# Kernel optimization log

Measured on AMD Instinct MI355X. Metric: run time of the kernel, lower is better.

The kernel has to match this reference:

```python
import jax, jax.numpy as jnp
import numpy as np

B, LQ = 16, 2048
EMB1, EMB2, HDIM, NHEAD = 1024, 768, 1024, 16


def setup_inputs() -> dict:
    key = jax.random.key(0)
    ks = jax.random.split(key, 8)
    s1 = 1.0 / np.sqrt(EMB1)
    s2 = 1.0 / np.sqrt(EMB2)
    return {
        "emb1": jax.random.normal(ks[0], (B, LQ, EMB1), jnp.float32),
        "emb2": jax.random.normal(ks[1], (B, EMB2), jnp.float32),
        "Wq": jax.random.uniform(ks[2], (HDIM, EMB1), jnp.float32, -s1, s1),
        "bq": jax.random.uniform(ks[3], (HDIM,), jnp.float32, -s1, s1),
        "Wk": jax.random.uniform(ks[4], (HDIM, EMB2), jnp.float32, -s2, s2),
        "bk": jax.random.uniform(ks[5], (HDIM,), jnp.float32, -s2, s2),
        "Wv": jax.random.uniform(ks[6], (HDIM, EMB2), jnp.float32, -s2, s2),
        "bv": jax.random.uniform(ks[7], (HDIM,), jnp.float32, -s2, s2),
        "n_head": NHEAD,
    }


def reference(emb1, emb2, Wq, bq, Wk, bk, Wv, bv, n_head):
    b, lq, _ = emb1.shape
    hdim = Wq.shape[0]
    dh = hdim // n_head
    # Q: [b, lq, hdim] -> [b, H, lq, dh]
    q = (jnp.einsum("bqe,he->bqh", emb1, Wq) + bq).reshape(b, lq, n_head, dh).transpose(0, 2, 1, 3)
    # K, V from per-batch vector: [b, hdim] -> [b, H, 1, dh]
    k = (emb2 @ Wk.T + bk).reshape(b, 1, n_head, dh).transpose(0, 2, 1, 3)
    v = (emb2 @ Wv.T + bv).reshape(b, 1, n_head, dh).transpose(0, 2, 1, 3)
    # att: [b, H, lq, 1] (no softmax, no scaling)
    att = jnp.einsum("bhqd,bhkd->bhqk", q, k)
    # sigmoid gate broadcast-multiplied with V: [b,H,lq,1]*[b,H,1,dh] -> [b,H,lq,dh]
    out = jax.nn.sigmoid(att) * v
    # back to [b, lq, hdim]; torch .squeeze(1) is a no-op for lq > 1
    return out.transpose(0, 2, 1, 3).reshape(b, lq, hdim)
```

## Files before the change

kernel.cpp:

```cpp
#include <hip/hip_runtime.h>
#include <hip/hip_fp16.h>
#include <cstdint>


typedef float    f4v __attribute__((ext_vector_type(4)));
typedef _Float16 h8v __attribute__((ext_vector_type(8)));

__global__ __launch_bounds__(256) void kv_kernel(
    const float* __restrict__ emb2, const float* __restrict__ Wk,
    const float* __restrict__ bk,   const float* __restrict__ Wv,
    const float* __restrict__ bv,   float* __restrict__ ws)
{
    const int kind  = blockIdx.y;
    const int htile = blockIdx.x;
    const float* W    = kind ? Wv : Wk;
    const float* bias = kind ? bv : bk;
    float* outp = ws + (kind ? 16384 : 0);

    const int t  = threadIdx.x;
    const int es = t >> 6;
    const int hl = (t >> 4) & 3;
    const int b  = t & 15;
    const int h  = htile * 4 + hl;

    const float4* W4 = (const float4*)(W + (size_t)h * 768) + es * 48;
    const float4* E4 = (const float4*)(emb2 + (size_t)b * 768) + es * 48;

    float acc = 0.f;
    #pragma unroll 8
    for (int j = 0; j < 48; ++j) {
        float4 w = W4[j];
        float4 a = E4[j];
        acc += w.x * a.x + w.y * a.y + w.z * a.z + w.w * a.w;
    }

    __shared__ float red[256];
    red[t] = acc;
    __syncthreads();
    if (t < 64) {
        float s = red[t] + red[t + 64] + red[t + 128] + red[t + 192] + bias[h];
        outp[b * 1024 + h] = s;
    }
}

__global__ __launch_bounds__(256) void fold_kernel(
    const float* __restrict__ Wq, const float* __restrict__ bq,
    float* __restrict__ ws)
{
    const int h = blockIdx.x;
    const int b = blockIdx.y;
    const float* kvec = ws;
    float* attb = ws + 32768;
    __half* wqk = (__half*)((char*)ws + 132096);

    const int t = threadIdx.x;
    __shared__ float kk[64];
    if (t < 64) {
        float kvl = kvec[b * 1024 + h * 64 + t];
        kk[t] = kvl;
        float s = kvl * bq[h * 64 + t];
        s += __shfl_xor(s, 1);  s += __shfl_xor(s, 2);
        s += __shfl_xor(s, 4);  s += __shfl_xor(s, 8);
        s += __shfl_xor(s, 16); s += __shfl_xor(s, 32);
        if (t == 0) attb[b * 16 + h] = s;
    }
    __syncthreads();

    float4 acc = make_float4(0.f, 0.f, 0.f, 0.f);
    const float4* Wrow = (const float4*)(Wq + (size_t)(h * 64) * 1024) + t;
    #pragma unroll 8
    for (int d = 0; d < 64; ++d) {
        float4 w = Wrow[(size_t)d * 256];
        float kd = kk[d];
        acc.x += kd * w.x; acc.y += kd * w.y;
        acc.z += kd * w.z; acc.w += kd * w.w;
    }
    union { __half2 h2[2]; uint2 u; } pk;
    pk.h2[0] = __floats2half2_rn(acc.x, acc.y);
    pk.h2[1] = __floats2half2_rn(acc.z, acc.w);
    *(uint2*)(wqk + (size_t)(b * 16 + h) * 1024 + t * 4) = pk.u;
}

__global__ __launch_bounds__(128) void att_kernel(
    const float* __restrict__ emb1, const float* __restrict__ ws,
    float* __restrict__ out)
{
    const int b    = blockIdx.y;
    const int t    = threadIdx.x;
    const int w    = t >> 6;
    const int lane = t & 63;
    const int q    = lane >> 4;
    const int m    = lane & 15;

    const int row0 = blockIdx.x * 32 + w * 16;

    const float*    vvec  = ws + 16384 + b * 1024;
    const float*    attbp = ws + 32768 + b * 16;
    const _Float16* wqk   = (const _Float16*)((const char*)ws + 132096)
                          + (size_t)b * 16384;

    const float*    Ap = emb1 + ((size_t)b * 2048 + row0 + m) * 1024 + q * 8;
    const _Float16* Bp = wqk + m * 1024 + q * 8;

    f4v acc = {0.f, 0.f, 0.f, 0.f};

    f4v a0 = *(const f4v*)(Ap);
    f4v a1 = *(const f4v*)(Ap + 4);
    h8v bf = *(const h8v*)(Bp);

    for (int c = 0; c < 32; ++c) {
        const int cn = (c < 31) ? c + 1 : 31;
        const float* An = Ap + cn * 32;
        f4v a0n = *(const f4v*)(An);
        f4v a1n = *(const f4v*)(An + 4);
        h8v bfn = *(const h8v*)(Bp + cn * 32);

        h8v af;
        af[0] = (_Float16)a0[0]; af[1] = (_Float16)a0[1];
        af[2] = (_Float16)a0[2]; af[3] = (_Float16)a0[3];
        af[4] = (_Float16)a1[0]; af[5] = (_Float16)a1[1];
        af[6] = (_Float16)a1[2]; af[7] = (_Float16)a1[3];

        acc = __builtin_amdgcn_mfma_f32_16x16x32_f16(af, bf, acc, 0, 0, 0);

        a0 = a0n; a1 = a1n; bf = bfn;
    }

    __shared__ float gl[2][16 * 17];
    float* g = gl[w];
    const float attb_l = attbp[m];
    #pragma unroll
    for (int j = 0; j < 4; ++j) {
        float att  = acc[j] + attb_l;
        float gate = 1.0f / (1.0f + __expf(-att));
        g[(q * 4 + j) * 17 + m] = gate;
    }
    __syncthreads();

    f4v vv[4];
    #pragma unroll
    for (int s = 0; s < 4; ++s)
        vv[s] = *(const f4v*)(vvec + s * 256 + lane * 4);

    float* Ob = out + ((size_t)b * 2048 + row0) * 1024 + lane * 4;
    #pragma unroll
    for (int r = 0; r < 16; ++r) {
        #pragma unroll
        for (int s = 0; s < 4; ++s) {
            float gg = g[r * 17 + s * 4 + q];
            f4v o = gg * vv[s];
            __builtin_nontemporal_store(o, (f4v*)(Ob + (size_t)r * 1024 + s * 256));
        }
    }
}

extern "C" void kernel_launch(void* const* d_in, const int* in_sizes, int n_in,
                              void* d_out, int out_size, void* d_ws, size_t ws_size,
                              hipStream_t stream) {
    const float* emb1 = (const float*)d_in[0];
    const float* emb2 = (const float*)d_in[1];
    const float* Wq   = (const float*)d_in[2];
    const float* bq   = (const float*)d_in[3];
    const float* Wk   = (const float*)d_in[4];
    const float* bk   = (const float*)d_in[5];
    const float* Wv   = (const float*)d_in[6];
    const float* bv   = (const float*)d_in[7];
    float* out = (float*)d_out;
    float* ws  = (float*)d_ws;

    kv_kernel  <<<dim3(256, 2), 256, 0, stream>>>(emb2, Wk, bk, Wv, bv, ws);
    fold_kernel<<<dim3(16, 16), 256, 0, stream>>>(Wq, bq, ws);
    att_kernel <<<dim3(64, 16), 128, 0, stream>>>(emb1, ws, out);
}
```

Baseline: 285.3 us.

## Split att_kernel K-reduction across four waves with all loads issued upfront

```diff
diff --git a/kernel.cpp b/kernel.cpp
--- a/kernel.cpp
+++ b/kernel.cpp
@@ -81,7 +81,7 @@
     *(uint2*)(wqk + (size_t)(b * 16 + h) * 1024 + t * 4) = pk.u;
 }
 
-__global__ __launch_bounds__(128) void att_kernel(
+__global__ __launch_bounds__(256, 4) void att_kernel(
     const float* __restrict__ emb1, const float* __restrict__ ws,
     float* __restrict__ out)
 {
@@ -92,7 +92,8 @@
     const int q    = lane >> 4;
     const int m    = lane & 15;
 
-    const int row0 = blockIdx.x * 32 + w * 16;
+    const int row0 = blockIdx.x * 16;
+    const int c0   = w * 8;
 
     const float*    vvec  = ws + 16384 + b * 1024;
     const float*    attbp = ws + 32768 + b * 16;
@@ -102,38 +103,43 @@
     const float*    Ap = emb1 + ((size_t)b * 2048 + row0 + m) * 1024 + q * 8;
     const _Float16* Bp = wqk + m * 1024 + q * 8;
 
+    f4v A0[8], A1[8];
+    h8v Bf[8];
+    #pragma unroll
+    for (int i = 0; i < 8; ++i) {
+        const float* ap = Ap + (c0 + i) * 32;
+        A0[i] = *(const f4v*)(ap);
+        A1[i] = *(const f4v*)(ap + 4);
+        Bf[i] = *(const h8v*)(Bp + (c0 + i) * 32);
+    }
+    __builtin_amdgcn_sched_barrier(0);
+
     f4v acc = {0.f, 0.f, 0.f, 0.f};
-
-    f4v a0 = *(const f4v*)(Ap);
-    f4v a1 = *(const f4v*)(Ap + 4);
-    h8v bf = *(const h8v*)(Bp);
-
-    for (int c = 0; c < 32; ++c) {
-        const int cn = (c < 31) ? c + 1 : 31;
-        const float* An = Ap + cn * 32;
-        f4v a0n = *(const f4v*)(An);
-        f4v a1n = *(const f4v*)(An + 4);
-        h8v bfn = *(const h8v*)(Bp + cn * 32);
-
+    #pragma unroll
+    for (int i = 0; i < 8; ++i) {
+        f4v a0 = A0[i], a1 = A1[i];
         h8v af;
         af[0] = (_Float16)a0[0]; af[1] = (_Float16)a0[1];
         af[2] = (_Float16)a0[2]; af[3] = (_Float16)a0[3];
         af[4] = (_Float16)a1[0]; af[5] = (_Float16)a1[1];
         af[6] = (_Float16)a1[2]; af[7] = (_Float16)a1[3];
-
-        acc = __builtin_amdgcn_mfma_f32_16x16x32_f16(af, bf, acc, 0, 0, 0);
-
-        a0 = a0n; a1 = a1n; bf = bfn;
+        acc = __builtin_amdgcn_mfma_f32_16x16x32_f16(af, Bf[i], acc, 0, 0, 0);
     }
 
-    __shared__ float gl[2][16 * 17];
-    float* g = gl[w];
-    const float attb_l = attbp[m];
-    #pragma unroll
-    for (int j = 0; j < 4; ++j) {
-        float att  = acc[j] + attb_l;
-        float gate = 1.0f / (1.0f + __expf(-att));
-        g[(q * 4 + j) * 17 + m] = gate;
+    __shared__ float sacc[4][16 * 17];
+    __shared__ float sg[16 * 17];
+    {
+        float* sa = sacc[w];
+        #pragma unroll
+        for (int j = 0; j < 4; ++j)
+            sa[(q * 4 + j) * 17 + m] = acc[j];
+    }
+    __syncthreads();
+    {
+        const int r = t >> 4, h = t & 15;
+        float s = sacc[0][r * 17 + h] + sacc[1][r * 17 + h]
+                + sacc[2][r * 17 + h] + sacc[3][r * 17 + h] + attbp[h];
+        sg[r * 17 + h] = 1.0f / (1.0f + __expf(-s));
     }
     __syncthreads();
 
@@ -144,10 +150,11 @@
 
     float* Ob = out + ((size_t)b * 2048 + row0) * 1024 + lane * 4;
     #pragma unroll
-    for (int r = 0; r < 16; ++r) {
+    for (int k = 0; k < 4; ++k) {
+        const int r = w * 4 + k;
         #pragma unroll
         for (int s = 0; s < 4; ++s) {
-            float gg = g[r * 17 + s * 4 + q];
+            float gg = sg[r * 17 + s * 4 + q];
             f4v o = gg * vv[s];
             __builtin_nontemporal_store(o, (f4v*)(Ob + (size_t)r * 1024 + s * 256));
         }
@@ -168,7 +175,7 @@
     float* out = (float*)d_out;
     float* ws  = (float*)d_ws;
 
-    kv_kernel  <<<dim3(256, 2), 256, 0, stream>>>(emb2, Wk, bk, Wv, bv, ws);
-    fold_kernel<<<dim3(16, 16), 256, 0, stream>>>(Wq, bq, ws);
-    att_kernel <<<dim3(64, 16), 128, 0, stream>>>(emb1, ws, out);
+    kv_kernel  <<<dim3(256, 2),  256, 0, stream>>>(emb2, Wk, bk, Wv, bv, ws);
+    fold_kernel<<<dim3(16, 16),  256, 0, stream>>>(Wq, bq, ws);
+    att_kernel <<<dim3(128, 16), 256, 0, stream>>>(emb1, ws, out);
 }
```

Result: faster. 274.5 us (-3.8%).
